# Kernel tuning notes

Hardware: AMD Instinct MI355X
Metric: run time of the kernel (lower is better)

Reference implementation:

```python
import jax, jax.numpy as jnp
import numpy as np

EPS = 1e-5  # torch.nn.LayerNorm default

def layernorm(x, gamma, beta):
    mu = jnp.mean(x, axis=-1, keepdims=True)
    var = jnp.mean(jnp.square(x - mu), axis=-1, keepdims=True)
    return (x - mu) * jax.lax.rsqrt(var + EPS) * gamma + beta

def setup_inputs() -> dict:
    key = jax.random.key(0)
    ks = jax.random.split(key, 5)
    B, H = 8192, 1024
    stdv = 1.0 / np.sqrt(H)
    inp = jax.random.normal(ks[0], (B, 4 * H), dtype=jnp.float32)
    hx = jax.random.normal(ks[1], (B, H), dtype=jnp.float32)
    cx = jax.random.normal(ks[2], (B, H), dtype=jnp.float32)
    weight_hh = jax.random.uniform(ks[3], (4 * H, H), dtype=jnp.float32, minval=-stdv, maxval=stdv)
    gamma_h = jnp.ones((4 * H,), jnp.float32)
    beta_h = jnp.zeros((4 * H,), jnp.float32)
    gamma_c = jnp.ones((H,), jnp.float32)
    beta_c = jnp.zeros((H,), jnp.float32)
    return {"input": inp, "hx": hx, "cx": cx, "weight_hh": weight_hh,
            "gamma_h": gamma_h, "beta_h": beta_h, "gamma_c": gamma_c, "beta_c": beta_c}

def reference(input, hx, cx, weight_hh, gamma_h, beta_h, gamma_c, beta_c):
    # hgates = LN(hx @ W_hh^T); gates = igates + hgates
    hgates = layernorm(jnp.matmul(hx, weight_hh.T), gamma_h, beta_h)
    gates = input + hgates  # [B, 4H]
    i_g, f_g, c_g, o_g = jnp.split(gates, 4, axis=1)
    ingate = jax.nn.sigmoid(i_g)
    forgetgate = jax.nn.sigmoid(f_g)
    cellgate = jnp.tanh(c_g)
    outgate = jax.nn.sigmoid(o_g)
    cy = layernorm(forgetgate * cx + ingate * cellgate, gamma_c, beta_c)
    hy = outgate * jnp.tanh(cy)
    return (hy, cy)
```

## Files before the change

### kernel.cpp

```cpp
#include <hip/hip_runtime.h>
#include <hip/hip_bf16.h>

typedef __attribute__((ext_vector_type(8))) short short8;
typedef __attribute__((ext_vector_type(4))) float f32x4;

#define LN_EPS 1e-5f

__device__ __forceinline__ ushort f32_to_bf16(float f) {
  union { float f; unsigned u; } v; v.f = f;
  unsigned u = v.u;
  u += 0x7FFFu + ((u >> 16) & 1u);
  return (ushort)(u >> 16);
}
__device__ __forceinline__ float bf16_to_f32(ushort h) {
  union { unsigned u; float f; } v; v.u = ((unsigned)h) << 16; return v.f;
}
__device__ __forceinline__ float sigmoid_f(float x) {
  return 1.0f / (1.0f + __expf(-x));
}
__device__ __forceinline__ float tanh_f(float x) {
  return 2.0f / (1.0f + __expf(-2.0f * x)) - 1.0f;
}

__device__ __forceinline__ void gload16(const ushort* g, ushort* l) {
  __builtin_amdgcn_global_load_lds(
      (const __attribute__((address_space(1))) unsigned int*)g,
      (__attribute__((address_space(3))) unsigned int*)l, 16, 0, 0);
}

__global__ __launch_bounds__(256) void cast2_f32_bf16(
    const float* __restrict__ a, ushort* __restrict__ oa, int na4,
    const float* __restrict__ b, ushort* __restrict__ ob, int nb4) {
  int i = blockIdx.x * 256 + threadIdx.x;
  int stride = gridDim.x * 256;
  for (; i < na4 + nb4; i += stride) {
    const float* src = (i < na4) ? a : b;
    ushort* dst = (i < na4) ? oa : ob;
    int k = (i < na4) ? i : i - na4;
    float4 v = ((const float4*)src)[k];
    ushort4 o;
    o.x = f32_to_bf16(v.x); o.y = f32_to_bf16(v.y);
    o.z = f32_to_bf16(v.z); o.w = f32_to_bf16(v.w);
    ((ushort4*)dst)[k] = o;
  }
}

__global__ __launch_bounds__(256) void gemm_bt(const ushort* __restrict__ A,
                                               const ushort* __restrict__ B,
                                               ushort* __restrict__ C,
                                               int M, int N, int K) {
  __shared__ alignas(16) ushort As[128 * 32];
  __shared__ alignas(16) ushort Bs[128 * 32];
  const int tid = threadIdx.x;
  const int lane = tid & 63;
  const int wave = tid >> 6;
  const int wm = wave >> 1, wn = wave & 1;
  const int bn = blockIdx.x, bm = blockIdx.y;

  f32x4 acc[4][4];
#pragma unroll
  for (int i = 0; i < 4; i++)
#pragma unroll
    for (int j = 0; j < 4; j++) acc[i][j] = (f32x4){0.f, 0.f, 0.f, 0.f};

  const int srow = tid >> 2;
  const int schunk = (tid & 3) ^ ((tid >> 3) & 3);
  const ushort* Ag = A + (size_t)(bm * 128 + srow) * K + schunk * 8;
  const ushort* Bg = B + (size_t)(bn * 128 + srow) * K + schunk * 8;
  ushort* Asl = As + tid * 8;
  ushort* Bsl = Bs + tid * 8;
  const size_t rowstep = (size_t)64 * K;

  const int frow = lane & 15;
  const int rchunk = (lane >> 4) ^ ((frow >> 1) & 3);
  int aoff[4], boff[4];
#pragma unroll
  for (int i = 0; i < 4; i++) {
    aoff[i] = (wm * 64 + i * 16 + frow) * 32 + rchunk * 8;
    boff[i] = (wn * 64 + i * 16 + frow) * 32 + rchunk * 8;
  }

  for (int k0 = 0; k0 < K; k0 += 32) {
    __syncthreads();
    gload16(Ag + k0, Asl);
    gload16(Ag + rowstep + k0, Asl + 2048);
    gload16(Bg + k0, Bsl);
    gload16(Bg + rowstep + k0, Bsl + 2048);
    __syncthreads();

    short8 af[4], bfr[4];
#pragma unroll
    for (int i = 0; i < 4; i++) af[i]  = *(const short8*)&As[aoff[i]];
#pragma unroll
    for (int j = 0; j < 4; j++) bfr[j] = *(const short8*)&Bs[boff[j]];
#pragma unroll
    for (int i = 0; i < 4; i++)
#pragma unroll
      for (int j = 0; j < 4; j++)
        acc[i][j] = __builtin_amdgcn_mfma_f32_16x16x32_bf16(af[i], bfr[j], acc[i][j], 0, 0, 0);
  }

  const int crow0 = bm * 128 + wm * 64;
  const int ccol0 = bn * 128 + wn * 64;
#pragma unroll
  for (int i = 0; i < 4; i++)
#pragma unroll
    for (int j = 0; j < 4; j++) {
      int col = ccol0 + j * 16 + (lane & 15);
      int rb = crow0 + i * 16 + ((lane >> 4) << 2);
#pragma unroll
      for (int r = 0; r < 4; r++)
        C[(size_t)(rb + r) * N + col] = f32_to_bf16(acc[i][j][r]);
    }
}

__global__ __launch_bounds__(256) void lstm_ln_kernel(
    const ushort* __restrict__ gates_pre,
    const float* __restrict__ input,
    const float* __restrict__ cx,
    const float* __restrict__ gamma_h, const float* __restrict__ beta_h,
    const float* __restrict__ gamma_c, const float* __restrict__ beta_c,
    float* __restrict__ hy, float* __restrict__ cy, int H) {
  const int FH = 4 * H;
  const int row = blockIdx.x;
  const int t = threadIdx.x;
  const int lane = t & 63, wv = t >> 6;
  const int j0 = t * 4;
  __shared__ float redA[8], redB[8];

  const ushort* gp = gates_pre + (size_t)row * FH;

  float xg[4][4];
  {
#pragma unroll
    for (int g = 0; g < 4; g++) {
      ushort4 u = *(const ushort4*)(gp + g * H + j0);
      xg[g][0] = bf16_to_f32(u.x); xg[g][1] = bf16_to_f32(u.y);
      xg[g][2] = bf16_to_f32(u.z); xg[g][3] = bf16_to_f32(u.w);
    }
  }

  float s1 = 0.f, s2 = 0.f;
#pragma unroll
  for (int g = 0; g < 4; g++)
#pragma unroll
    for (int q = 0; q < 4; q++) { s1 += xg[g][q]; s2 += xg[g][q] * xg[g][q]; }
  {
    float a = s1, b = s2;
#pragma unroll
    for (int off = 32; off > 0; off >>= 1) {
      a += __shfl_down(a, off, 64);
      b += __shfl_down(b, off, 64);
    }
    if (lane == 0) { redA[wv] = a; redA[4 + wv] = b; }
  }
  __syncthreads();
  const float inv_fh = 1.0f / (float)FH;
  const float mu  = (redA[0] + redA[1] + redA[2] + redA[3]) * inv_fh;
  const float m2  = (redA[4] + redA[5] + redA[6] + redA[7]) * inv_fh;
  const float rstd = rsqrtf(m2 - mu * mu + LN_EPS);

  const float* ip = input + (size_t)row * FH;
  float a_g[4][4];
#pragma unroll
  for (int g = 0; g < 4; g++) {
    float4 iv = *(const float4*)(ip + g * H + j0);
    float4 gv = *(const float4*)(gamma_h + g * H + j0);
    float4 bv = *(const float4*)(beta_h + g * H + j0);
    a_g[g][0] = (xg[g][0] - mu) * rstd * gv.x + bv.x + iv.x;
    a_g[g][1] = (xg[g][1] - mu) * rstd * gv.y + bv.y + iv.y;
    a_g[g][2] = (xg[g][2] - mu) * rstd * gv.z + bv.z + iv.z;
    a_g[g][3] = (xg[g][3] - mu) * rstd * gv.w + bv.w + iv.w;
  }

  float4 cxv = *(const float4*)(cx + (size_t)row * H + j0);
  const float* cxa = (const float*)&cxv;
  float cell[4], og[4];
  float s3 = 0.f, s4 = 0.f;
#pragma unroll
  for (int q = 0; q < 4; q++) {
    float in_s = sigmoid_f(a_g[0][q]);
    float fg_s = sigmoid_f(a_g[1][q]);
    float cg_t = tanh_f(a_g[2][q]);
    og[q] = sigmoid_f(a_g[3][q]);
    float cl = fg_s * cxa[q] + in_s * cg_t;
    cell[q] = cl;
    s3 += cl; s4 += cl * cl;
  }
  {
    float a = s3, b = s4;
#pragma unroll
    for (int off = 32; off > 0; off >>= 1) {
      a += __shfl_down(a, off, 64);
      b += __shfl_down(b, off, 64);
    }
    if (lane == 0) { redB[wv] = a; redB[4 + wv] = b; }
  }
  __syncthreads();
  const float inv_h = 1.0f / (float)H;
  const float mu2   = (redB[0] + redB[1] + redB[2] + redB[3]) * inv_h;
  const float m22   = (redB[4] + redB[5] + redB[6] + redB[7]) * inv_h;
  const float rstd2 = rsqrtf(m22 - mu2 * mu2 + LN_EPS);

  float4 gc = *(const float4*)(gamma_c + j0);
  float4 bc = *(const float4*)(beta_c + j0);
  const float* gca = (const float*)&gc;
  const float* bca = (const float*)&bc;
  float4 cyo, hyo;
  float* cyp = (float*)&cyo; float* hyp = (float*)&hyo;
#pragma unroll
  for (int q = 0; q < 4; q++) {
    float cyv = (cell[q] - mu2) * rstd2 * gca[q] + bca[q];
    cyp[q] = cyv;
    hyp[q] = og[q] * tanh_f(cyv);
  }
  *(float4*)(cy + (size_t)row * H + j0) = cyo;
  *(float4*)(hy + (size_t)row * H + j0) = hyo;
}

extern "C" void kernel_launch(void* const* d_in, const int* in_sizes, int n_in,
                              void* d_out, int out_size, void* d_ws, size_t ws_size,
                              hipStream_t stream) {
  (void)n_in; (void)out_size; (void)ws_size;
  const float* input   = (const float*)d_in[0];
  const float* hx      = (const float*)d_in[1];
  const float* cx      = (const float*)d_in[2];
  const float* w       = (const float*)d_in[3];
  const float* gamma_h = (const float*)d_in[4];
  const float* beta_h  = (const float*)d_in[5];
  const float* gamma_c = (const float*)d_in[6];
  const float* beta_c  = (const float*)d_in[7];

  const int H  = in_sizes[6];
  const int B  = in_sizes[1] / H;
  const int FH = 4 * H;
  const int K  = H;

  ushort* hx_bf = (ushort*)d_ws;
  ushort* w_bf  = hx_bf + (size_t)B * K;
  ushort* gates = w_bf + (size_t)FH * K;

  float* hy = (float*)d_out;
  float* cy = hy + (size_t)B * H;

  cast2_f32_bf16<<<2048, 256, 0, stream>>>(hx, hx_bf, (B * K) / 4,
                                           w, w_bf, (FH * K) / 4);

  dim3 grid(FH / 128, B / 128);
  gemm_bt<<<grid, 256, 0, stream>>>(hx_bf, w_bf, gates, B, FH, K);

  lstm_ln_kernel<<<B, 256, 0, stream>>>(gates, input, cx, gamma_h, beta_h,
                                        gamma_c, beta_c, hy, cy, H);
}
```

Before: 366.0 us.

## Rewrite GEMM as 256x256 double-buffered tile with phased MFMA scheduling

Replaces the 128x128 single-buffered bf16 GEMM with a 256x256 tile, 512-thread, K=64-step kernel. The next K tile is prefetched into a second LDS buffer while the current one is consumed, and the MFMAs are split into four barrier-separated phases with raised wave priority. The kernel also adds an XCD-aware block index swizzle and a wider LDS XOR swizzle. This aims to hide global-load latency and raise data reuse per tile, at the cost of 128KB of LDS per block, higher register pressure, and fewer blocks (512) for the GPU to spread across its compute units.

```diff
diff --git a/kernel.cpp b/kernel.cpp
--- a/kernel.cpp
+++ b/kernel.cpp
@@ -45,73 +45,121 @@
   }
 }
 
-__global__ __launch_bounds__(256) void gemm_bt(const ushort* __restrict__ A,
-                                               const ushort* __restrict__ B,
-                                               ushort* __restrict__ C,
-                                               int M, int N, int K) {
-  __shared__ alignas(16) ushort As[128 * 32];
-  __shared__ alignas(16) ushort Bs[128 * 32];
+#define DS_A(QM)                                                            \
+  _Pragma("unroll") for (int ks = 0; ks < 2; ks++)                          \
+  _Pragma("unroll") for (int m = 0; m < 4; m++)                             \
+    af[ks][m] = *(const short8*)&Acur[aoff[ks] + (QM) * 4096 + m * 1024];
+#define DS_B(QN)                                                            \
+  _Pragma("unroll") for (int ks = 0; ks < 2; ks++)                          \
+  _Pragma("unroll") for (int n = 0; n < 2; n++)                             \
+    bf_[ks][n] = *(const short8*)&Bcur[boff[ks] + (QN) * 2048 + n * 1024];
+#define MFMAS(QM, QN)                                                       \
+  _Pragma("unroll") for (int ks = 0; ks < 2; ks++)                          \
+  _Pragma("unroll") for (int m = 0; m < 4; m++)                             \
+  _Pragma("unroll") for (int n = 0; n < 2; n++)                             \
+    acc[(QM) * 4 + m][(QN) * 2 + n] = __builtin_amdgcn_mfma_f32_16x16x32_bf16( \
+        af[ks][m], bf_[ks][n], acc[(QM) * 4 + m][(QN) * 2 + n], 0, 0, 0);
+#define PHASE_SYNC_PRE()                                                    \
+  __builtin_amdgcn_s_barrier();                                             \
+  asm volatile("s_waitcnt lgkmcnt(0)" ::: "memory");                        \
+  __builtin_amdgcn_sched_barrier(0);                                        \
+  __builtin_amdgcn_s_setprio(1);
+#define PHASE_SYNC_POST()                                                   \
+  __builtin_amdgcn_s_setprio(0);                                            \
+  __builtin_amdgcn_s_barrier();
+
+__global__ __launch_bounds__(512, 2) void gemm_bt(const ushort* __restrict__ A,
+                                                  const ushort* __restrict__ B,
+                                                  ushort* __restrict__ C,
+                                                  int M, int N, int K) {
+  __shared__ alignas(16) ushort lds[65536];
   const int tid = threadIdx.x;
-  const int lane = tid & 63;
-  const int wave = tid >> 6;
-  const int wm = wave >> 1, wn = wave & 1;
-  const int bn = blockIdx.x, bm = blockIdx.y;
-
-  f32x4 acc[4][4];
-#pragma unroll
-  for (int i = 0; i < 4; i++)
+  const int l = tid & 63;
+  const int wv = tid >> 6;
+  const int wm = wv >> 2, wn = wv & 3;
+
+  const int nwg = gridDim.x;
+  const int cpx = nwg >> 3;
+  const int bid = blockIdx.x;
+  const int swz = (bid & 7) * cpx + (bid >> 3);
+  const int nbn = N >> 8;
+  const int bm = swz / nbn;
+  const int bn = swz % nbn;
+
+  f32x4 acc[8][4];
+#pragma unroll
+  for (int i = 0; i < 8; i++)
 #pragma unroll
     for (int j = 0; j < 4; j++) acc[i][j] = (f32x4){0.f, 0.f, 0.f, 0.f};
 
-  const int srow = tid >> 2;
-  const int schunk = (tid & 3) ^ ((tid >> 3) & 3);
-  const ushort* Ag = A + (size_t)(bm * 128 + srow) * K + schunk * 8;
-  const ushort* Bg = B + (size_t)(bn * 128 + srow) * K + schunk * 8;
-  ushort* Asl = As + tid * 8;
-  ushort* Bsl = Bs + tid * 8;
-  const size_t rowstep = (size_t)64 * K;
-
-  const int frow = lane & 15;
-  const int rchunk = (lane >> 4) ^ ((frow >> 1) & 3);
-  int aoff[4], boff[4];
-#pragma unroll
-  for (int i = 0; i < 4; i++) {
-    aoff[i] = (wm * 64 + i * 16 + frow) * 32 + rchunk * 8;
-    boff[i] = (wn * 64 + i * 16 + frow) * 32 + rchunk * 8;
-  }
-
-  for (int k0 = 0; k0 < K; k0 += 32) {
-    __syncthreads();
-    gload16(Ag + k0, Asl);
-    gload16(Ag + rowstep + k0, Asl + 2048);
-    gload16(Bg + k0, Bsl);
-    gload16(Bg + rowstep + k0, Bsl + 2048);
-    __syncthreads();
-
-    short8 af[4], bfr[4];
-#pragma unroll
-    for (int i = 0; i < 4; i++) af[i]  = *(const short8*)&As[aoff[i]];
-#pragma unroll
-    for (int j = 0; j < 4; j++) bfr[j] = *(const short8*)&Bs[boff[j]];
-#pragma unroll
-    for (int i = 0; i < 4; i++)
-#pragma unroll
-      for (int j = 0; j < 4; j++)
-        acc[i][j] = __builtin_amdgcn_mfma_f32_16x16x32_bf16(af[i], bfr[j], acc[i][j], 0, 0, 0);
-  }
-
-  const int crow0 = bm * 128 + wm * 64;
-  const int ccol0 = bn * 128 + wn * 64;
-#pragma unroll
-  for (int i = 0; i < 4; i++)
-#pragma unroll
-    for (int j = 0; j < 4; j++) {
-      int col = ccol0 + j * 16 + (lane & 15);
-      int rb = crow0 + i * 16 + ((lane >> 4) << 2);
+  const int lc = (tid & 7) ^ ((tid >> 3) & 7);
+  const ushort* srcA0 = A + (size_t)(bm * 256 + (tid >> 3)) * K + lc * 8;
+  const ushort* srcB0 = B + (size_t)(bn * 256 + (tid >> 3)) * K + lc * 8;
+  ushort* dstA0 = lds + tid * 8;
+  ushort* dstB0 = lds + 32768 + tid * 8;
+#define STAGE(BUFSEL, KCOL)                                                 \
+  _Pragma("unroll") for (int l2 = 0; l2 < 4; l2++) {                        \
+    gload16(srcA0 + (size_t)l2 * 64 * K + (KCOL), dstA0 + (BUFSEL) * 16384 + l2 * 4096); \
+    gload16(srcB0 + (size_t)l2 * 64 * K + (KCOL), dstB0 + (BUFSEL) * 16384 + l2 * 4096); \
+  }
+
+  const int lr = l & 15;
+  const int lg = l >> 4;
+  const int lx = l & 7;
+  int aoff[2], boff[2];
+#pragma unroll
+  for (int ks = 0; ks < 2; ks++) {
+    const int pc = ((ks << 2) | lg) ^ lx;
+    aoff[ks] = (wm * 128 + lr) * 64 + pc * 8;
+    boff[ks] = (wn * 64 + lr) * 64 + pc * 8;
+  }
+
+  STAGE(0, 0);
+  asm volatile("s_waitcnt vmcnt(0)" ::: "memory");
+  __builtin_amdgcn_s_barrier();
+
+  const int NT = K >> 6;
+  for (int t = 0; t < NT; ++t) {
+    const ushort* Acur = lds + (t & 1) * 16384;
+    const ushort* Bcur = lds + 32768 + (t & 1) * 16384;
+    const int nbuf = (t & 1) ^ 1;
+    short8 af[2][4], bf_[2][2];
+
+    DS_A(0); DS_B(0);
+    if (t < NT - 1) { STAGE(nbuf, (t + 1) * 64); }
+    PHASE_SYNC_PRE();
+    MFMAS(0, 0);
+    PHASE_SYNC_POST();
+
+    DS_B(1);
+    PHASE_SYNC_PRE();
+    MFMAS(0, 1);
+    PHASE_SYNC_POST();
+
+    DS_A(1);
+    PHASE_SYNC_PRE();
+    MFMAS(1, 1);
+    PHASE_SYNC_POST();
+
+    DS_B(0);
+    PHASE_SYNC_PRE();
+    MFMAS(1, 0);
+    __builtin_amdgcn_s_setprio(0);
+    asm volatile("s_waitcnt vmcnt(0)" ::: "memory");
+    __builtin_amdgcn_s_barrier();
+  }
+
+#pragma unroll
+  for (int mi = 0; mi < 8; mi++) {
+    const int rowb = bm * 256 + wm * 128 + mi * 16 + lg * 4;
+#pragma unroll
+    for (int ni = 0; ni < 4; ni++) {
+      const int col = bn * 256 + wn * 64 + ni * 16 + lr;
 #pragma unroll
       for (int r = 0; r < 4; r++)
-        C[(size_t)(rb + r) * N + col] = f32_to_bf16(acc[i][j][r]);
+        C[(size_t)(rowb + r) * N + col] = f32_to_bf16(acc[mi][ni][r]);
     }
+  }
 }
 
 __global__ __launch_bounds__(256) void lstm_ln_kernel(
@@ -131,13 +179,11 @@
   const ushort* gp = gates_pre + (size_t)row * FH;
 
   float xg[4][4];
-  {
-#pragma unroll
-    for (int g = 0; g < 4; g++) {
-      ushort4 u = *(const ushort4*)(gp + g * H + j0);
-      xg[g][0] = bf16_to_f32(u.x); xg[g][1] = bf16_to_f32(u.y);
-      xg[g][2] = bf16_to_f32(u.z); xg[g][3] = bf16_to_f32(u.w);
-    }
+#pragma unroll
+  for (int g = 0; g < 4; g++) {
+    ushort4 u = *(const ushort4*)(gp + g * H + j0);
+    xg[g][0] = bf16_to_f32(u.x); xg[g][1] = bf16_to_f32(u.y);
+    xg[g][2] = bf16_to_f32(u.z); xg[g][3] = bf16_to_f32(u.w);
   }
 
   float s1 = 0.f, s2 = 0.f;
@@ -246,8 +292,8 @@
   cast2_f32_bf16<<<2048, 256, 0, stream>>>(hx, hx_bf, (B * K) / 4,
                                            w, w_bf, (FH * K) / 4);
 
-  dim3 grid(FH / 128, B / 128);
-  gemm_bt<<<grid, 256, 0, stream>>>(hx_bf, w_bf, gates, B, FH, K);
+  const int nblocks = (B / 256) * (FH / 256);
+  gemm_bt<<<nblocks, 512, 0, stream>>>(hx_bf, w_bf, gates, B, FH, K);
 
   lstm_ln_kernel<<<B, 256, 0, stream>>>(gates, input, cx, gamma_h, beta_h,
                                         gamma_c, beta_c, hy, cy, H);
```

Measured after the change: 350.8 us. 4.2% less time.
